# Optimization experiments

Hardware: AMD Instinct MI355X
Metric: run time of the kernel (lower is better)

The kernel has to match this reference:

```python
import jax, jax.numpy as jnp
import numpy as np

N = 100000      # nodes
E = 1600000     # edges (avg degree 16)
F_IN = 128      # node feature dim
F_OUT = 128     # GCN output dim


def setup_inputs() -> dict:
    key = jax.random.key(0)
    ks = jax.random.split(key, 11)
    s = 0.05  # weight scale to keep activations sane
    return {
        "x": jax.random.normal(ks[0], (N, F_IN), jnp.float32),
        "edge_index": jax.random.randint(ks[1], (2, E), 0, N, jnp.int32),
        "W": jax.random.normal(ks[2], (F_IN, F_OUT), jnp.float32) * s,
        "p": jax.random.normal(ks[3], (F_IN,), jnp.float32),
        "w_ih": jax.random.normal(ks[4], (3 * F_OUT, F_IN), jnp.float32) * s,
        "w_hh": jax.random.normal(ks[5], (3 * F_OUT, F_OUT), jnp.float32) * s,
        "b_ih": jax.random.normal(ks[6], (3 * F_OUT,), jnp.float32) * s,
        "b_hh": jax.random.normal(ks[7], (3 * F_OUT,), jnp.float32) * s,
        "conv_bias": jax.random.normal(ks[8], (F_OUT,), jnp.float32) * s,
        "lin_w": jax.random.normal(ks[9], (1, F_OUT), jnp.float32) * s,
        "lin_b": jax.random.normal(ks[10], (1,), jnp.float32) * s,
    }


def reference(x, edge_index, W, p, w_ih, w_hh, b_ih, b_hh, conv_bias, lin_w, lin_b):
    n_nodes = x.shape[0]
    k, H = W.shape  # k = F_IN rows, H = F_OUT hidden size

    # --- TopK summarize: pick k nodes, gate by tanh(score) -> X_tilde [k, F_IN]
    scores = x @ p / jnp.linalg.norm(p)
    top_vals, top_idx = jax.lax.top_k(scores, k)
    x_tilde = x[top_idx] * jnp.tanh(top_vals)[:, None]

    # --- one GRU step evolving W (hidden state = rows of W)
    gi = x_tilde @ w_ih.T + b_ih   # [k, 3H]
    gh = W @ w_hh.T + b_hh         # [k, 3H]
    r = jax.nn.sigmoid(gi[:, :H] + gh[:, :H])
    z = jax.nn.sigmoid(gi[:, H:2 * H] + gh[:, H:2 * H])
    n = jnp.tanh(gi[:, 2 * H:] + r * gh[:, 2 * H:])
    W_new = (1.0 - z) * n + z * W  # [F_IN, F_OUT]

    # --- GCN conv with fixed W: sym-normalized adjacency with self loops
    row, col = edge_index[0], edge_index[1]
    deg = jax.ops.segment_sum(jnp.ones_like(row, dtype=x.dtype), col,
                              num_segments=n_nodes) + 1.0  # +1 for self loop
    dinv = jax.lax.rsqrt(deg)
    xw = x @ W_new                                   # [N, F_OUT]
    coef = dinv[row] * dinv[col]                     # [E]
    agg = jax.ops.segment_sum(xw[row] * coef[:, None], col, num_segments=n_nodes)
    agg = agg + xw * (dinv * dinv)[:, None] + conv_bias  # self-loop term + bias

    # --- head: ReLU + Linear(F_OUT, 1)
    h = jax.nn.relu(agg)
    return h @ lin_w.T + lin_b  # [N, 1]
```

## Files before the change

### kernel.cpp

```cpp
#include <hip/hip_runtime.h>
#include <math.h>

#define N_NODES 100000
#define N_EDGES 1600000
#define F 128

#define BSH 8
#define NBUCK 391
#define BCAP 5120
#define PB_EDGES 2048
#define NB_PART 782
#define NB_SCORES 1563
#define NB_COLLECT 392

typedef unsigned int u32;
typedef unsigned short u16;
typedef __attribute__((ext_vector_type(8))) short short8;
typedef __attribute__((ext_vector_type(4))) float floatx4;
typedef __attribute__((ext_vector_type(2))) float f32x2;
typedef __attribute__((ext_vector_type(4))) u32 u32x4;


__device__ __forceinline__ u32 key_of(float s) {
    u32 u = __float_as_uint(s);
    return (u & 0x80000000u) ? ~u : (u | 0x80000000u);
}

__device__ __forceinline__ float wave_reduce(float v) {
    #pragma unroll
    for (int off = 32; off > 0; off >>= 1) v += __shfl_down(v, off, 64);
    return v;
}

__device__ __forceinline__ u16 f2bf(float f) {
    u32 u = __float_as_uint(f);
    u += 0x7fffu + ((u >> 16) & 1u);
    return (u16)(u >> 16);
}

__device__ __forceinline__ float bflo(u32 b) { return __uint_as_float(b << 16); }
__device__ __forceinline__ float bfhi(u32 b) { return __uint_as_float(b & 0xffff0000u); }

__device__ __forceinline__ void pk_acc(f32x2& acc, u32 u) {
    f32x2 v; v.x = bflo(u); v.y = bfhi(u);
    asm("v_pk_add_f32 %0, %1, %0" : "+v"(acc) : "v"(v));
}
__device__ __forceinline__ void pk_add2(f32x2& a, f32x2 b) {
    asm("v_pk_add_f32 %0, %1, %0" : "+v"(a) : "v"(b));
}


__global__ __launch_bounds__(256) void k_part(const int* __restrict__ ei,
                                              u32* __restrict__ gcur,
                                              u32* __restrict__ pairs) {
    __shared__ u32 lh[NBUCK];
    __shared__ u32 lbase[NBUCK];
    int t = threadIdx.x;
    int e0 = blockIdx.x * PB_EDGES;
    int e1 = e0 + PB_EDGES; if (e1 > N_EDGES) e1 = N_EDGES;
    for (int i = t; i < NBUCK; i += 256) lh[i] = 0u;
    __syncthreads();
    for (int e = e0 + t; e < e1; e += 256)
        atomicAdd(&lh[((u32)ei[N_EDGES + e]) >> BSH], 1u);
    __syncthreads();
    for (int b = t; b < NBUCK; b += 256) {
        u32 c = lh[b];
        lbase[b] = c ? atomicAdd(&gcur[b], c) : 0u;
        lh[b] = 0u;
    }
    __syncthreads();
    for (int e = e0 + t; e < e1; e += 256) {
        u32 d = (u32)ei[N_EDGES + e];
        u32 b = d >> BSH;
        u32 pos = lbase[b] + atomicAdd(&lh[b], 1u);
        pairs[(size_t)b * BCAP + pos] = ((d & 255u) << 17) | (u32)ei[e];
    }
}


__global__ __launch_bounds__(256) void k_scores(const float* __restrict__ x,
                                                const float* __restrict__ p,
                                                float* __restrict__ scores,
                                                u32* __restrict__ hist16,
                                                u32* __restrict__ xb) {
    int sb = blockIdx.x;
    int wave = threadIdx.x >> 6;
    int lane = threadIdx.x & 63;
    int q = lane >> 4, sub = lane & 15;
    int nb0 = sb * 64 + wave * 16 + q;
    float4 p0 = *(const float4*)&p[sub * 8];
    float4 p1 = *(const float4*)&p[sub * 8 + 4];
    float4 v0[4], v1[4];
    if (nb0 + 12 < N_NODES) {
        #pragma unroll
        for (int r = 0; r < 4; r++) {
            const float* xr = &x[(size_t)(nb0 + r * 4) * F + sub * 8];
            v0[r] = *(const float4*)xr;
            v1[r] = *(const float4*)(xr + 4);
        }
    } else {
        #pragma unroll
        for (int r = 0; r < 4; r++) {
            int node = nb0 + r * 4;
            v0[r] = make_float4(0.f, 0.f, 0.f, 0.f);
            v1[r] = make_float4(0.f, 0.f, 0.f, 0.f);
            if (node < N_NODES) {
                const float* xr = &x[(size_t)node * F + sub * 8];
                v0[r] = *(const float4*)xr;
                v1[r] = *(const float4*)(xr + 4);
            }
        }
    }
    #pragma unroll
    for (int r = 0; r < 4; r++) {
        int node = nb0 + r * 4;
        if (node >= N_NODES) continue;
        if (xb) {
            u32x4 pk;
            pk.x = (u32)f2bf(v0[r].x) | ((u32)f2bf(v0[r].y) << 16);
            pk.y = (u32)f2bf(v0[r].z) | ((u32)f2bf(v0[r].w) << 16);
            pk.z = (u32)f2bf(v1[r].x) | ((u32)f2bf(v1[r].y) << 16);
            pk.w = (u32)f2bf(v1[r].z) | ((u32)f2bf(v1[r].w) << 16);
            *(u32x4*)&xb[(size_t)node * 64 + sub * 4] = pk;
        }
        float d = v0[r].x * p0.x + v0[r].y * p0.y + v0[r].z * p0.z + v0[r].w * p0.w
                + v1[r].x * p1.x + v1[r].y * p1.y + v1[r].z * p1.z + v1[r].w * p1.w;
        #pragma unroll
        for (int off = 1; off < 16; off <<= 1) d += __shfl_xor(d, off, 64);
        if (sub == 0) {
            scores[node] = d;
            atomicAdd(&hist16[key_of(d) >> 16], 1u);
        }
    }
}


__global__ __launch_bounds__(1024) void k_scan16(const u32* __restrict__ hist16,
                                                 u32* __restrict__ state,
                                                 const u32* __restrict__ gcur,
                                                 u32* __restrict__ bbase) {
    __shared__ u32 a[1024];
    int t = threadIdx.x;
    if (blockIdx.x == 0) {
        const uint4* h4 = (const uint4*)hist16;
        u32 local = 0;
        #pragma unroll
        for (int i = 0; i < 16; i++) {
            uint4 v = h4[t * 16 + i];
            local += v.x + v.y + v.z + v.w;
        }
        a[t] = local;
        __syncthreads();
        for (int off = 1; off < 1024; off <<= 1) {
            u32 add = (t + off < 1024) ? a[t + off] : 0u;
            __syncthreads();
            a[t] += add;
            __syncthreads();
        }
        u32 S_above = (t == 1023) ? 0u : a[t + 1];
        if (S_above < 128u && a[t] >= 128u) {
            u32 cum = S_above;
            for (int v = t * 64 + 63; v >= t * 64; v--) {
                cum += hist16[v];
                if (cum >= 128u) { state[0] = (u32)v; break; }
            }
        }
    } else {
        u32 v = (t < NBUCK) ? gcur[t] : 0u;
        a[t] = v;
        __syncthreads();
        for (int off = 1; off < 1024; off <<= 1) {
            u32 add = (t >= off) ? a[t - off] : 0u;
            __syncthreads();
            a[t] += add;
            __syncthreads();
        }
        if (t < NBUCK) bbase[t] = a[t] - v;
    }
}


__global__ __launch_bounds__(256) void k_mid(const float* __restrict__ scores,
                                             u32* __restrict__ state,
                                             u32* __restrict__ cand,
                                             const u32* __restrict__ pairs,
                                             const u32* __restrict__ gcur,
                                             const u32* __restrict__ bbase,
                                             u32* __restrict__ offs,
                                             float* __restrict__ dinv,
                                             u32* __restrict__ ebuf) {
    if (blockIdx.x < NB_COLLECT) {
        u32 T = state[0] << 16;
        int i = blockIdx.x * 256 + threadIdx.x;
        if (i < N_NODES) {
            if (key_of(scores[i]) >= T) {
                u32 pos = atomicAdd(&state[2], 1u);
                if (pos < 2048u) cand[pos] = (u32)i;
            }
        }
    } else {
        __shared__ u32 h[256];
        __shared__ u32 sc[256];
        int b = blockIdx.x - NB_COLLECT, t = threadIdx.x;
        u32 base = bbase[b];
        u32 cnt  = gcur[b];
        const u32* seg = pairs + (size_t)b * BCAP;
        u32 lo = (u32)b << BSH;
        h[t] = 0u;
        __syncthreads();
        for (u32 i = t; i < cnt; i += 256)
            atomicAdd(&h[seg[i] >> 17], 1u);
        __syncthreads();
        sc[t] = h[t];
        __syncthreads();
        for (int off = 1; off < 256; off <<= 1) {
            u32 v = (t >= off) ? sc[t - off] : 0u;
            __syncthreads();
            sc[t] += v;
            __syncthreads();
        }
        int nn = N_NODES - (int)lo;
        if (t < nn) {
            u32 c = h[t];
            offs[lo + t] = base + (sc[t] - c);
            dinv[lo + t] = rsqrtf((float)c + 1.0f);
        }
        u32 excl = sc[t] - h[t];
        __syncthreads();
        sc[t] = excl;
        __syncthreads();
        for (u32 i = t; i < cnt; i += 256) {
            u32 pr = seg[i];
            u32 pos = base + atomicAdd(&sc[pr >> 17], 1u);
            ebuf[pos] = pr & 0x1ffffu;
        }
        if (b == 0 && t == 0) offs[N_NODES] = N_EDGES;
    }
}


__global__ __launch_bounds__(256) void k_ggemm(const float* __restrict__ x,
                                               const float* __restrict__ W,
                                               const float* __restrict__ w_ih,
                                               const float* __restrict__ w_hh,
                                               const float* __restrict__ scores,
                                               const float* __restrict__ p,
                                               const u32* __restrict__ state,
                                               const u32* __restrict__ cand,
                                               float* __restrict__ G) {
    __shared__ float As[32][128];
    __shared__ float Bs[64][131];
    __shared__ u32 s_topi[128];
    __shared__ float s_gate[128];
    __shared__ float s_inv;
    int t = threadIdx.x;
    u32*   ci  = (u32*)&Bs[0][0];
    float* csc = (float*)&Bs[16][0];
    if (t < 64) {
        float2 pv = *(const float2*)&p[t * 2];
        float d = pv.x * pv.x + pv.y * pv.y;
        d = wave_reduce(d);
        if (t == 0) s_inv = rsqrtf(d);
    }
    u32 nc = state[2]; if (nc > 2048u) nc = 2048u;
    for (u32 i = t; i < nc; i += 256) { u32 ix = cand[i]; ci[i] = ix; csc[i] = scores[ix]; }
    __syncthreads();
    for (u32 i = t; i < nc; i += 256) {
        u32 myk = key_of(csc[i]);
        u32 myi = ci[i];
        int rank = 0;
        for (u32 j = 0; j < nc; j++) {
            u32 ok = key_of(csc[j]);
            rank += (int)((ok > myk) || (ok == myk && ci[j] < myi));
        }
        if (rank < 128) {
            s_topi[rank] = myi;
            s_gate[rank] = tanhf(csc[i] * s_inv);
        }
    }
    __syncthreads();

    int k0 = blockIdx.x * 32;
    int by = blockIdx.y;
    int j0 = by * 64;
    bool is_gi = (by < 6);
    #pragma unroll
    for (int i = 0; i < 4; i++) {
        int l = t + i * 256;
        int row = l >> 5, c4 = l & 31;
        float4 v;
        if (is_gi) {
            u32 idx = s_topi[k0 + row];
            float gt = s_gate[k0 + row];
            v = *(const float4*)&x[(size_t)idx * F + c4 * 4];
            v.x *= gt; v.y *= gt; v.z *= gt; v.w *= gt;
        } else {
            v = *(const float4*)&W[(k0 + row) * F + c4 * 4];
        }
        *(float4*)&As[row][c4 * 4] = v;
    }
    const float* mat = is_gi ? w_ih : w_hh;
    int jbase = is_gi ? j0 : (j0 - 384);
    #pragma unroll
    for (int i = 0; i < 8; i++) {
        int l = t + i * 256;
        int row = l >> 5, c4 = l & 31;
        float4 v = *(const float4*)&mat[(jbase + row) * F + c4 * 4];
        Bs[row][c4 * 4 + 0] = v.x; Bs[row][c4 * 4 + 1] = v.y;
        Bs[row][c4 * 4 + 2] = v.z; Bs[row][c4 * 4 + 3] = v.w;
    }
    __syncthreads();
    int ty = t >> 5, tx = t & 31;
    float acc[4][2] = {};
    #pragma unroll 4
    for (int f = 0; f < 128; f++) {
        float b0 = Bs[tx * 2][f], b1 = Bs[tx * 2 + 1][f];
        #pragma unroll
        for (int i = 0; i < 4; i++) {
            float a = As[ty * 4 + i][f];
            acc[i][0] += a * b0;
            acc[i][1] += a * b1;
        }
    }
    #pragma unroll
    for (int i = 0; i < 4; i++) {
        int k = k0 + ty * 4 + i;
        G[(size_t)k * 768 + j0 + tx * 2 + 0] = acc[i][0];
        G[(size_t)k * 768 + j0 + tx * 2 + 1] = acc[i][1];
    }
}


__global__ void k_gate(const float* __restrict__ G, const float* __restrict__ W,
                       const float* __restrict__ b_ih, const float* __restrict__ b_hh,
                       float* __restrict__ Wnew, u16* __restrict__ Bfrag) {
    int idx = blockIdx.x * blockDim.x + threadIdx.x;
    int k = idx >> 7, h = idx & 127;
    const float* gk = &G[(size_t)k * 768];
    float gir = gk[h]       + b_ih[h];
    float giz = gk[128 + h] + b_ih[128 + h];
    float gin = gk[256 + h] + b_ih[256 + h];
    float ghr = gk[384 + h] + b_hh[h];
    float ghz = gk[512 + h] + b_hh[128 + h];
    float ghn = gk[640 + h] + b_hh[256 + h];
    float wv  = W[k * F + h];
    float rg = 1.0f / (1.0f + expf(-(gir + ghr)));
    float z  = 1.0f / (1.0f + expf(-(giz + ghz)));
    float n  = tanhf(gin + rg * ghn);
    float val = (1.0f - z) * n + z * wv;
    Wnew[k * F + h] = val;
    int nb = h >> 4, kc = k >> 5, q = (k >> 3) & 3, m = h & 15, jj = k & 7;
    Bfrag[(((nb * 4 + kc) * 64) + q * 16 + m) * 8 + jj] = f2bf(val);
}


__device__ __forceinline__ void gemm_core(u16* As, const u16* __restrict__ Bfrag,
                                          const float* __restrict__ dinv,
                                          u16* __restrict__ yw, int r0, int t) {
    int wv = t >> 6, lane = t & 63;
    int q = lane >> 4, m = lane & 15;
    floatx4 acc[8] = {};
    #pragma unroll
    for (int kc = 0; kc < 4; kc++) {
        short8 a = *(const short8*)&As[((wv * 4 + kc) * 64 + lane) * 8];
        #pragma unroll
        for (int nb = 0; nb < 8; nb++) {
            short8 bfr = *(const short8*)&Bfrag[((nb * 4 + kc) * 64 + lane) * 8];
            acc[nb] = __builtin_amdgcn_mfma_f32_16x16x32_bf16(a, bfr, acc[nb], 0, 0, 0);
        }
    }
    __syncthreads();

    float d[4];
    #pragma unroll
    for (int reg = 0; reg < 4; reg++) {
        int gr = r0 + wv * 16 + q * 4 + reg;
        d[reg] = (gr < N_NODES) ? dinv[gr] : 0.f;
    }
    #pragma unroll
    for (int nb = 0; nb < 8; nb++) {
        #pragma unroll
        for (int reg = 0; reg < 4; reg++) {
            int row = wv * 16 + q * 4 + reg;
            As[row * 132 + nb * 16 + m] = f2bf(acc[nb][reg] * d[reg]);
        }
    }
    __syncthreads();
    {
        int row = t >> 2, segi = t & 3;
        int gr = r0 + row;
        if (gr < N_NODES) {
            const uint2* src = (const uint2*)&As[row * 132 + segi * 32];
            uint2* dst = (uint2*)&yw[(size_t)gr * F + segi * 32];
            #pragma unroll
            for (int i = 0; i < 8; i++) dst[i] = src[i];
        }
    }
}

__global__ __launch_bounds__(256) void k_gemm(const float* __restrict__ x,
                                              const u16* __restrict__ Bfrag,
                                              const float* __restrict__ dinv,
                                              u16* __restrict__ yw) {
    __shared__ __align__(16) u16 As[8448];
    int t = threadIdx.x;
    int r0 = blockIdx.x * 64;
    #pragma unroll
    for (int i = 0; i < 8; i++) {
        int l = t + i * 256;
        int row = l >> 5, c4 = l & 31;
        int f0 = c4 * 4;
        float4 v = {0.f, 0.f, 0.f, 0.f};
        if (r0 + row < N_NODES) v = *(const float4*)&x[(size_t)(r0 + row) * F + f0];
        int widx = (((row >> 4) * 4 + (f0 >> 5)) * 64 + ((f0 >> 3) & 3) * 16 + (row & 15)) * 8
                   + (f0 & 7);
        ushort4 s4;
        s4.x = f2bf(v.x); s4.y = f2bf(v.y); s4.z = f2bf(v.z); s4.w = f2bf(v.w);
        *(ushort4*)&As[widx] = s4;
    }
    __syncthreads();
    gemm_core(As, Bfrag, dinv, yw, r0, t);
}

__global__ __launch_bounds__(256) void k_gemm_xb(const u32* __restrict__ xb,
                                                 const u16* __restrict__ Bfrag,
                                                 const float* __restrict__ dinv,
                                                 u16* __restrict__ yw) {
    __shared__ __align__(16) u16 As[8448];
    int t = threadIdx.x;
    int r0 = blockIdx.x * 64;
    #pragma unroll
    for (int i = 0; i < 4; i++) {
        int wdx = t + i * 256;
        int lane = wdx & 63, chunk = wdx >> 6;
        int kc = chunk & 3, rowhi = chunk >> 2;
        int q = lane >> 4, m = lane & 15;
        int row = rowhi * 16 + m;
        u32x4 v = {0u, 0u, 0u, 0u};
        if (r0 + row < N_NODES)
            v = *(const u32x4*)&xb[(size_t)(r0 + row) * 64 + kc * 16 + q * 4];
        *(u32x4*)&As[wdx * 8] = v;
    }
    __syncthreads();
    gemm_core(As, Bfrag, dinv, yw, r0, t);
}


#define EDGE_GROUP(J) {                                                      \
    u32 r = ebuf[(J) + q];                                                   \
    uint4 bb = *(const uint4*)&yw32[(size_t)r * 64 + sub * 4];               \
    pk_acc(a01, bb.x); pk_acc(a23, bb.y);                                    \
    pk_acc(a45, bb.z); pk_acc(a67, bb.w); }

#define BFLY(A) {                                                            \
    f32x2 tb;                                                                \
    tb.x = __shfl_xor(A.x, 16, 64); tb.y = __shfl_xor(A.y, 16, 64);          \
    pk_add2(A, tb);                                                          \
    tb.x = __shfl_xor(A.x, 32, 64); tb.y = __shfl_xor(A.y, 32, 64);          \
    pk_add2(A, tb); }

__global__ void k_gather(const u32* __restrict__ yw32, const u32* __restrict__ offs,
                         const u32* __restrict__ ebuf, const float* __restrict__ dinv,
                         const float* __restrict__ conv_bias, const float* __restrict__ lin_w,
                         const float* __restrict__ lin_b, float* __restrict__ out,
                         int node0) {
    int c = node0 + blockIdx.x * 4 + (threadIdx.x >> 6);
    if (c >= N_NODES) return;
    int lane = threadIdx.x & 63;
    int q = lane >> 4, sub = lane & 15;
    u32 jbeg = offs[c], jend = offs[c + 1];
    f32x2 a01 = {0.f, 0.f}, a23 = {0.f, 0.f}, a45 = {0.f, 0.f}, a67 = {0.f, 0.f};
    u32 j = jbeg;
    for (; j + 16 <= jend; j += 16) {
        EDGE_GROUP(j) EDGE_GROUP(j + 4) EDGE_GROUP(j + 8) EDGE_GROUP(j + 12)
    }
    for (; j + 4 <= jend; j += 4) EDGE_GROUP(j)
    u32 rem = jend - j;
    if (rem) {
        u32 idx = ((u32)q < rem) ? (j + q) : j;
        u32 r = ebuf[idx];
        uint4 bb = *(const uint4*)&yw32[(size_t)r * 64 + sub * 4];
        if ((u32)q < rem) {
            pk_acc(a01, bb.x); pk_acc(a23, bb.y);
            pk_acc(a45, bb.z); pk_acc(a67, bb.w);
        }
    }
    BFLY(a01) BFLY(a23) BFLY(a45) BFLY(a67)
    float dc = dinv[c];
    uint4 sb = *(const uint4*)&yw32[(size_t)c * 64 + sub * 4];
    float4 cb0 = *(const float4*)&conv_bias[sub * 8];
    float4 cb1 = *(const float4*)&conv_bias[sub * 8 + 4];
    float4 lw0 = *(const float4*)&lin_w[sub * 8];
    float4 lw1 = *(const float4*)&lin_w[sub * 8 + 4];
    float h0 = fmaxf(dc * (a01.x + bflo(sb.x)) + cb0.x, 0.f);
    float h1 = fmaxf(dc * (a01.y + bfhi(sb.x)) + cb0.y, 0.f);
    float h2 = fmaxf(dc * (a23.x + bflo(sb.y)) + cb0.z, 0.f);
    float h3 = fmaxf(dc * (a23.y + bfhi(sb.y)) + cb0.w, 0.f);
    float h4 = fmaxf(dc * (a45.x + bflo(sb.z)) + cb1.x, 0.f);
    float h5 = fmaxf(dc * (a45.y + bfhi(sb.z)) + cb1.y, 0.f);
    float h6 = fmaxf(dc * (a67.x + bflo(sb.w)) + cb1.z, 0.f);
    float h7 = fmaxf(dc * (a67.y + bfhi(sb.w)) + cb1.w, 0.f);
    float part = (h0 * lw0.x + h1 * lw0.y + h2 * lw0.z + h3 * lw0.w)
               + (h4 * lw1.x + h5 * lw1.y + h6 * lw1.z + h7 * lw1.w);
    #pragma unroll
    for (int off = 8; off > 0; off >>= 1) part += __shfl_down(part, off, 64);
    if (lane == 0) out[c] = part + lin_b[0];
}


extern "C" void kernel_launch(void* const* d_in, const int* in_sizes, int n_in,
                              void* d_out, int out_size, void* d_ws, size_t ws_size,
                              hipStream_t stream) {
    const float* x         = (const float*)d_in[0];
    const int*   ei        = (const int*)  d_in[1];
    const float* W         = (const float*)d_in[2];
    const float* p         = (const float*)d_in[3];
    const float* w_ih      = (const float*)d_in[4];
    const float* w_hh      = (const float*)d_in[5];
    const float* b_ih      = (const float*)d_in[6];
    const float* b_hh      = (const float*)d_in[7];
    const float* conv_bias = (const float*)d_in[8];
    const float* lin_w     = (const float*)d_in[9];
    const float* lin_b     = (const float*)d_in[10];
    float* out = (float*)d_out;

    u32*   w  = (u32*)d_ws;
    float* wf = (float*)d_ws;

    const size_t SCORES_W = 0;
    const size_t DINV_W   = 100096;
    const size_t OFFS_W   = 200192;
    const size_t HIST16_W = 300288;
    const size_t STATE_W  = 365824;
    const size_t GCUR_W   = 365832;
    const size_t BBASE_W  = 366224;
    const size_t CAND_W   = 366616;
    const size_t WNEW_W   = 368920;
    const size_t BFRAG_W  = 385304;
    const size_t PAIRS_W  = 389400;
    const size_t EBUF_W   = 2400000;
    const size_t YW_W     = 4000000;
    const size_t XB_W     = 10400000;

    float* scores  = wf + SCORES_W;
    float* dinv    = wf + DINV_W;
    u32*   offs    = w  + OFFS_W;
    u32*   hist16  = w  + HIST16_W;
    u32*   state   = w  + STATE_W;
    u32*   gcur    = w  + GCUR_W;
    u32*   bbase   = w  + BBASE_W;
    u32*   cand    = w  + CAND_W;
    float* Wnew    = wf + WNEW_W;
    u16*   Bfrag   = (u16*)(w + BFRAG_W);
    u32*   pairs   = w  + PAIRS_W;
    float* G       = wf + PAIRS_W;
    u32*   ebuf    = w  + EBUF_W;
    u16*   yw      = (u16*)(w + YW_W);
    u32*   yw32    = w + YW_W;

    bool   use_xb  = ws_size >= (XB_W + 6400000) * sizeof(u32);
    u32*   xb      = use_xb ? (w + XB_W) : (u32*)0;

    hipMemsetAsync(hist16, 0, (65536 + 8 + NBUCK) * sizeof(u32), stream);

    k_part<<<NB_PART, 256, 0, stream>>>(ei, gcur, pairs);
    k_scores<<<NB_SCORES, 256, 0, stream>>>(x, p, scores, hist16, xb);
    k_scan16<<<2, 1024, 0, stream>>>(hist16, state, gcur, bbase);
    k_mid<<<NB_COLLECT + NBUCK, 256, 0, stream>>>(scores, state, cand, pairs, gcur,
                                                  bbase, offs, dinv, ebuf);
    k_ggemm<<<dim3(4, 12), 256, 0, stream>>>(x, W, w_ih, w_hh, scores, p, state,
                                             cand, G);
    k_gate<<<64, 256, 0, stream>>>(G, W, b_ih, b_hh, Wnew, Bfrag);

    if (use_xb) k_gemm_xb<<<1563, 256, 0, stream>>>(xb, Bfrag, dinv, yw);
    else        k_gemm   <<<1563, 256, 0, stream>>>(x,  Bfrag, dinv, yw);

    k_gather<<<6250, 256, 0, stream>>>(yw32, offs, ebuf, dinv, conv_bias, lin_w,
                                       lin_b, out, 0);
    k_gather<<<6250, 256, 0, stream>>>(yw32, offs, ebuf, dinv, conv_bias, lin_w,
                                       lin_b, out, 25000);
    k_gather<<<6250, 256, 0, stream>>>(yw32, offs, ebuf, dinv, conv_bias, lin_w,
                                       lin_b, out, 50000);
    k_gather<<<6250, 256, 0, stream>>>(yw32, offs, ebuf, dinv, conv_bias, lin_w,
                                       lin_b, out, 75000);
}
```

Measured before the change: 346.1 us.

## Fuse edge partition with score pass, drop bf16 x copy, single gather launch

Merges the edge bucketing kernel and the score/histogram kernel into one launch whose blocks branch on block index, so both independent front-end stages can run concurrently. Removes the bf16 staging copy of x written during scoring, so the GEMM now reads fp32 x directly and converts it itself. The four quarter-sized gather launches become one launch over all nodes. This trades the extra bf16 write and later reread for a larger fp32 read in the GEMM, and cuts launch count.

```diff
diff --git a/kernel.cpp b/kernel.cpp
--- a/kernel.cpp
+++ b/kernel.cpp
@@ -18,7 +18,6 @@
 typedef __attribute__((ext_vector_type(8))) short short8;
 typedef __attribute__((ext_vector_type(4))) float floatx4;
 typedef __attribute__((ext_vector_type(2))) float f32x2;
-typedef __attribute__((ext_vector_type(4))) u32 u32x4;
 
 
 __device__ __forceinline__ u32 key_of(float s) {
@@ -50,86 +49,97 @@
 }
 
 
-__global__ __launch_bounds__(256) void k_part(const int* __restrict__ ei,
-                                              u32* __restrict__ gcur,
-                                              u32* __restrict__ pairs) {
-    __shared__ u32 lh[NBUCK];
-    __shared__ u32 lbase[NBUCK];
-    int t = threadIdx.x;
-    int e0 = blockIdx.x * PB_EDGES;
-    int e1 = e0 + PB_EDGES; if (e1 > N_EDGES) e1 = N_EDGES;
-    for (int i = t; i < NBUCK; i += 256) lh[i] = 0u;
-    __syncthreads();
-    for (int e = e0 + t; e < e1; e += 256)
-        atomicAdd(&lh[((u32)ei[N_EDGES + e]) >> BSH], 1u);
-    __syncthreads();
-    for (int b = t; b < NBUCK; b += 256) {
-        u32 c = lh[b];
-        lbase[b] = c ? atomicAdd(&gcur[b], c) : 0u;
-        lh[b] = 0u;
-    }
-    __syncthreads();
-    for (int e = e0 + t; e < e1; e += 256) {
-        u32 d = (u32)ei[N_EDGES + e];
-        u32 b = d >> BSH;
-        u32 pos = lbase[b] + atomicAdd(&lh[b], 1u);
-        pairs[(size_t)b * BCAP + pos] = ((d & 255u) << 17) | (u32)ei[e];
-    }
-}
-
-
-__global__ __launch_bounds__(256) void k_scores(const float* __restrict__ x,
-                                                const float* __restrict__ p,
-                                                float* __restrict__ scores,
-                                                u32* __restrict__ hist16,
-                                                u32* __restrict__ xb) {
-    int sb = blockIdx.x;
-    int wave = threadIdx.x >> 6;
-    int lane = threadIdx.x & 63;
-    int q = lane >> 4, sub = lane & 15;
-    int nb0 = sb * 64 + wave * 16 + q;
-    float4 p0 = *(const float4*)&p[sub * 8];
-    float4 p1 = *(const float4*)&p[sub * 8 + 4];
-    float4 v0[4], v1[4];
-    if (nb0 + 12 < N_NODES) {
-        #pragma unroll
-        for (int r = 0; r < 4; r++) {
-            const float* xr = &x[(size_t)(nb0 + r * 4) * F + sub * 8];
-            v0[r] = *(const float4*)xr;
-            v1[r] = *(const float4*)(xr + 4);
+__global__ __launch_bounds__(256, 4)
+void k_front(const float* __restrict__ x, const float* __restrict__ p,
+             const int* __restrict__ ei, float* __restrict__ scores,
+             u32* __restrict__ hist16, u32* __restrict__ gcur,
+             u32* __restrict__ pairs) {
+    if (blockIdx.x < NB_PART) {
+        __shared__ u32 lh[NBUCK];
+        __shared__ u32 lbase[NBUCK];
+        int t = threadIdx.x;
+        int e0 = blockIdx.x * PB_EDGES;
+        int e1 = e0 + PB_EDGES; if (e1 > N_EDGES) e1 = N_EDGES;
+        for (int i = t; i < NBUCK; i += 256) lh[i] = 0u;
+        __syncthreads();
+        for (int e = e0 + t; e < e1; e += 256)
+            atomicAdd(&lh[((u32)ei[N_EDGES + e]) >> BSH], 1u);
+        __syncthreads();
+        for (int b = t; b < NBUCK; b += 256) {
+            u32 c = lh[b];
+            lbase[b] = c ? atomicAdd(&gcur[b], c) : 0u;
+            lh[b] = 0u;
+        }
+        __syncthreads();
+        for (int e = e0 + t; e < e1; e += 256) {
+            u32 d = (u32)ei[N_EDGES + e];
+            u32 b = d >> BSH;
+            u32 pos = lbase[b] + atomicAdd(&lh[b], 1u);
+            pairs[(size_t)b * BCAP + pos] = ((d & 255u) << 17) | (u32)ei[e];
         }
     } else {
-        #pragma unroll
-        for (int r = 0; r < 4; r++) {
-            int node = nb0 + r * 4;
-            v0[r] = make_float4(0.f, 0.f, 0.f, 0.f);
-            v1[r] = make_float4(0.f, 0.f, 0.f, 0.f);
-            if (node < N_NODES) {
+        int sb = blockIdx.x - NB_PART;
+        int wave = threadIdx.x >> 6;
+        int lane = threadIdx.x & 63;
+        int q = lane >> 4, sub = lane & 15;
+        int nb0 = sb * 64 + wave * 16 + q;
+        float4 p0 = *(const float4*)&p[sub * 8];
+        float4 p1 = *(const float4*)&p[sub * 8 + 4];
+        if (nb0 + 12 < N_NODES) {
+            const float* x0 = &x[(size_t)(nb0     ) * F + sub * 8];
+            const float* x1 = &x[(size_t)(nb0 +  4) * F + sub * 8];
+            const float* x2 = &x[(size_t)(nb0 +  8) * F + sub * 8];
+            const float* x3 = &x[(size_t)(nb0 + 12) * F + sub * 8];
+            float4 a0 = *(const float4*)x0;
+            float4 b0 = *(const float4*)(x0 + 4);
+            float4 a1 = *(const float4*)x1;
+            float4 b1 = *(const float4*)(x1 + 4);
+            float4 a2 = *(const float4*)x2;
+            float4 b2 = *(const float4*)(x2 + 4);
+            float4 a3 = *(const float4*)x3;
+            float4 b3 = *(const float4*)(x3 + 4);
+            float d0 = a0.x * p0.x + a0.y * p0.y + a0.z * p0.z + a0.w * p0.w
+                     + b0.x * p1.x + b0.y * p1.y + b0.z * p1.z + b0.w * p1.w;
+            float d1 = a1.x * p0.x + a1.y * p0.y + a1.z * p0.z + a1.w * p0.w
+                     + b1.x * p1.x + b1.y * p1.y + b1.z * p1.z + b1.w * p1.w;
+            float d2 = a2.x * p0.x + a2.y * p0.y + a2.z * p0.z + a2.w * p0.w
+                     + b2.x * p1.x + b2.y * p1.y + b2.z * p1.z + b2.w * p1.w;
+            float d3 = a3.x * p0.x + a3.y * p0.y + a3.z * p0.z + a3.w * p0.w
+                     + b3.x * p1.x + b3.y * p1.y + b3.z * p1.z + b3.w * p1.w;
+            #pragma unroll
+            for (int off = 1; off < 16; off <<= 1) {
+                d0 += __shfl_xor(d0, off, 64);
+                d1 += __shfl_xor(d1, off, 64);
+                d2 += __shfl_xor(d2, off, 64);
+                d3 += __shfl_xor(d3, off, 64);
+            }
+            if (sub == 0) {
+                scores[nb0]      = d0;
+                scores[nb0 + 4]  = d1;
+                scores[nb0 + 8]  = d2;
+                scores[nb0 + 12] = d3;
+                atomicAdd(&hist16[key_of(d0) >> 16], 1u);
+                atomicAdd(&hist16[key_of(d1) >> 16], 1u);
+                atomicAdd(&hist16[key_of(d2) >> 16], 1u);
+                atomicAdd(&hist16[key_of(d3) >> 16], 1u);
+            }
+        } else {
+            #pragma unroll
+            for (int r = 0; r < 4; r++) {
+                int node = nb0 + r * 4;
+                if (node >= N_NODES) continue;
                 const float* xr = &x[(size_t)node * F + sub * 8];
-                v0[r] = *(const float4*)xr;
-                v1[r] = *(const float4*)(xr + 4);
+                float4 v0 = *(const float4*)xr;
+                float4 v1 = *(const float4*)(xr + 4);
+                float d = v0.x * p0.x + v0.y * p0.y + v0.z * p0.z + v0.w * p0.w
+                        + v1.x * p1.x + v1.y * p1.y + v1.z * p1.z + v1.w * p1.w;
+                #pragma unroll
+                for (int off = 1; off < 16; off <<= 1) d += __shfl_xor(d, off, 64);
+                if (sub == 0) {
+                    scores[node] = d;
+                    atomicAdd(&hist16[key_of(d) >> 16], 1u);
+                }
             }
-        }
-    }
-    #pragma unroll
-    for (int r = 0; r < 4; r++) {
-        int node = nb0 + r * 4;
-        if (node >= N_NODES) continue;
-        if (xb) {
-            u32x4 pk;
-            pk.x = (u32)f2bf(v0[r].x) | ((u32)f2bf(v0[r].y) << 16);
-            pk.y = (u32)f2bf(v0[r].z) | ((u32)f2bf(v0[r].w) << 16);
-            pk.z = (u32)f2bf(v1[r].x) | ((u32)f2bf(v1[r].y) << 16);
-            pk.w = (u32)f2bf(v1[r].z) | ((u32)f2bf(v1[r].w) << 16);
-            *(u32x4*)&xb[(size_t)node * 64 + sub * 4] = pk;
-        }
-        float d = v0[r].x * p0.x + v0[r].y * p0.y + v0[r].z * p0.z + v0[r].w * p0.w
-                + v1[r].x * p1.x + v1[r].y * p1.y + v1[r].z * p1.z + v1[r].w * p1.w;
-        #pragma unroll
-        for (int off = 1; off < 16; off <<= 1) d += __shfl_xor(d, off, 64);
-        if (sub == 0) {
-            scores[node] = d;
-            atomicAdd(&hist16[key_of(d) >> 16], 1u);
         }
     }
 }
@@ -354,50 +364,6 @@
 }
 
 
-__device__ __forceinline__ void gemm_core(u16* As, const u16* __restrict__ Bfrag,
-                                          const float* __restrict__ dinv,
-                                          u16* __restrict__ yw, int r0, int t) {
-    int wv = t >> 6, lane = t & 63;
-    int q = lane >> 4, m = lane & 15;
-    floatx4 acc[8] = {};
-    #pragma unroll
-    for (int kc = 0; kc < 4; kc++) {
-        short8 a = *(const short8*)&As[((wv * 4 + kc) * 64 + lane) * 8];
-        #pragma unroll
-        for (int nb = 0; nb < 8; nb++) {
-            short8 bfr = *(const short8*)&Bfrag[((nb * 4 + kc) * 64 + lane) * 8];
-            acc[nb] = __builtin_amdgcn_mfma_f32_16x16x32_bf16(a, bfr, acc[nb], 0, 0, 0);
-        }
-    }
-    __syncthreads();
-
-    float d[4];
-    #pragma unroll
-    for (int reg = 0; reg < 4; reg++) {
-        int gr = r0 + wv * 16 + q * 4 + reg;
-        d[reg] = (gr < N_NODES) ? dinv[gr] : 0.f;
-    }
-    #pragma unroll
-    for (int nb = 0; nb < 8; nb++) {
-        #pragma unroll
-        for (int reg = 0; reg < 4; reg++) {
-            int row = wv * 16 + q * 4 + reg;
-            As[row * 132 + nb * 16 + m] = f2bf(acc[nb][reg] * d[reg]);
-        }
-    }
-    __syncthreads();
-    {
-        int row = t >> 2, segi = t & 3;
-        int gr = r0 + row;
-        if (gr < N_NODES) {
-            const uint2* src = (const uint2*)&As[row * 132 + segi * 32];
-            uint2* dst = (uint2*)&yw[(size_t)gr * F + segi * 32];
-            #pragma unroll
-            for (int i = 0; i < 8; i++) dst[i] = src[i];
-        }
-    }
-}
-
 __global__ __launch_bounds__(256) void k_gemm(const float* __restrict__ x,
                                               const u16* __restrict__ Bfrag,
                                               const float* __restrict__ dinv,
@@ -419,30 +385,46 @@
         *(ushort4*)&As[widx] = s4;
     }
     __syncthreads();
-    gemm_core(As, Bfrag, dinv, yw, r0, t);
-}
-
-__global__ __launch_bounds__(256) void k_gemm_xb(const u32* __restrict__ xb,
-                                                 const u16* __restrict__ Bfrag,
-                                                 const float* __restrict__ dinv,
-                                                 u16* __restrict__ yw) {
-    __shared__ __align__(16) u16 As[8448];
-    int t = threadIdx.x;
-    int r0 = blockIdx.x * 64;
-    #pragma unroll
-    for (int i = 0; i < 4; i++) {
-        int wdx = t + i * 256;
-        int lane = wdx & 63, chunk = wdx >> 6;
-        int kc = chunk & 3, rowhi = chunk >> 2;
-        int q = lane >> 4, m = lane & 15;
-        int row = rowhi * 16 + m;
-        u32x4 v = {0u, 0u, 0u, 0u};
-        if (r0 + row < N_NODES)
-            v = *(const u32x4*)&xb[(size_t)(r0 + row) * 64 + kc * 16 + q * 4];
-        *(u32x4*)&As[wdx * 8] = v;
+
+    int wv = t >> 6, lane = t & 63;
+    int q = lane >> 4, m = lane & 15;
+    floatx4 acc[8] = {};
+    #pragma unroll
+    for (int kc = 0; kc < 4; kc++) {
+        short8 a = *(const short8*)&As[((wv * 4 + kc) * 64 + lane) * 8];
+        #pragma unroll
+        for (int nb = 0; nb < 8; nb++) {
+            short8 bfr = *(const short8*)&Bfrag[((nb * 4 + kc) * 64 + lane) * 8];
+            acc[nb] = __builtin_amdgcn_mfma_f32_16x16x32_bf16(a, bfr, acc[nb], 0, 0, 0);
+        }
     }
     __syncthreads();
-    gemm_core(As, Bfrag, dinv, yw, r0, t);
+
+    float d[4];
+    #pragma unroll
+    for (int reg = 0; reg < 4; reg++) {
+        int gr = r0 + wv * 16 + q * 4 + reg;
+        d[reg] = (gr < N_NODES) ? dinv[gr] : 0.f;
+    }
+    #pragma unroll
+    for (int nb = 0; nb < 8; nb++) {
+        #pragma unroll
+        for (int reg = 0; reg < 4; reg++) {
+            int row = wv * 16 + q * 4 + reg;
+            As[row * 132 + nb * 16 + m] = f2bf(acc[nb][reg] * d[reg]);
+        }
+    }
+    __syncthreads();
+    {
+        int row = t >> 2, segi = t & 3;
+        int gr = r0 + row;
+        if (gr < N_NODES) {
+            const uint2* src = (const uint2*)&As[row * 132 + segi * 32];
+            uint2* dst = (uint2*)&yw[(size_t)gr * F + segi * 32];
+            #pragma unroll
+            for (int i = 0; i < 8; i++) dst[i] = src[i];
+        }
+    }
 }
 
 
@@ -462,9 +444,8 @@
 __global__ void k_gather(const u32* __restrict__ yw32, const u32* __restrict__ offs,
                          const u32* __restrict__ ebuf, const float* __restrict__ dinv,
                          const float* __restrict__ conv_bias, const float* __restrict__ lin_w,
-                         const float* __restrict__ lin_b, float* __restrict__ out,
-                         int node0) {
-    int c = node0 + blockIdx.x * 4 + (threadIdx.x >> 6);
+                         const float* __restrict__ lin_b, float* __restrict__ out) {
+    int c = blockIdx.x * 4 + (threadIdx.x >> 6);
     if (c >= N_NODES) return;
     int lane = threadIdx.x & 63;
     int q = lane >> 4, sub = lane & 15;
@@ -540,7 +521,6 @@
     const size_t PAIRS_W  = 389400;
     const size_t EBUF_W   = 2400000;
     const size_t YW_W     = 4000000;
-    const size_t XB_W     = 10400000;
 
     float* scores  = wf + SCORES_W;
     float* dinv    = wf + DINV_W;
@@ -558,13 +538,10 @@
     u16*   yw      = (u16*)(w + YW_W);
     u32*   yw32    = w + YW_W;
 
-    bool   use_xb  = ws_size >= (XB_W + 6400000) * sizeof(u32);
-    u32*   xb      = use_xb ? (w + XB_W) : (u32*)0;
-
     hipMemsetAsync(hist16, 0, (65536 + 8 + NBUCK) * sizeof(u32), stream);
 
-    k_part<<<NB_PART, 256, 0, stream>>>(ei, gcur, pairs);
-    k_scores<<<NB_SCORES, 256, 0, stream>>>(x, p, scores, hist16, xb);
+    k_front<<<NB_PART + NB_SCORES, 256, 0, stream>>>(x, p, ei, scores, hist16,
+                                                     gcur, pairs);
     k_scan16<<<2, 1024, 0, stream>>>(hist16, state, gcur, bbase);
     k_mid<<<NB_COLLECT + NBUCK, 256, 0, stream>>>(scores, state, cand, pairs, gcur,
                                                   bbase, offs, dinv, ebuf);
@@ -572,15 +549,8 @@
                                              cand, G);
     k_gate<<<64, 256, 0, stream>>>(G, W, b_ih, b_hh, Wnew, Bfrag);
 
-    if (use_xb) k_gemm_xb<<<1563, 256, 0, stream>>>(xb, Bfrag, dinv, yw);
-    else        k_gemm   <<<1563, 256, 0, stream>>>(x,  Bfrag, dinv, yw);
-
-    k_gather<<<6250, 256, 0, stream>>>(yw32, offs, ebuf, dinv, conv_bias, lin_w,
-                                       lin_b, out, 0);
-    k_gather<<<6250, 256, 0, stream>>>(yw32, offs, ebuf, dinv, conv_bias, lin_w,
-                                       lin_b, out, 25000);
-    k_gather<<<6250, 256, 0, stream>>>(yw32, offs, ebuf, dinv, conv_bias, lin_w,
-                                       lin_b, out, 50000);
-    k_gather<<<6250, 256, 0, stream>>>(yw32, offs, ebuf, dinv, conv_bias, lin_w,
-                                       lin_b, out, 75000);
-}
+    k_gemm<<<1563, 256, 0, stream>>>(x, Bfrag, dinv, yw);
+
+    k_gather<<<25000, 256, 0, stream>>>(yw32, offs, ebuf, dinv, conv_bias, lin_w,
+                                        lin_b, out);
+}
```

New measurement: 298.6 us. 13.7% less time.
